# Kernel optimization log

Hardware: AMD Instinct MI355X
Metric: run time of the kernel (lower is better)

Reference implementation:

```python
import jax, jax.numpy as jnp
import numpy as np

GRID_SIZE = 5
SPLINE_ORDER = 3
GRID_RANGE = (-1.0, 1.0)
KERNEL = 3
N_CONVS = 8


def make_grid():
    # Matches KANLinear: arange(-K, G+K+1) * h + grid_range[0]
    h = (GRID_RANGE[1] - GRID_RANGE[0]) / GRID_SIZE
    return jnp.arange(-SPLINE_ORDER, GRID_SIZE + SPLINE_ORDER + 1, dtype=jnp.float32) * h + GRID_RANGE[0]


def b_splines(x, grid):
    # x: (..., kk) -> bases: (..., kk, grid_size + spline_order)
    x = x[..., None]
    bases = ((x >= grid[:-1]) & (x < grid[1:])).astype(x.dtype)
    for p in range(1, SPLINE_ORDER + 1):
        left = (x - grid[: -(p + 1)]) / (grid[p:-1] - grid[: -(p + 1)])
        right = (grid[p + 1:] - x) / (grid[p + 1:] - grid[1:-p])
        bases = left * bases[..., :-1] + right * bases[..., 1:]
    return bases


def setup_inputs() -> dict:
    key = jax.random.key(0)
    k1, k2, k3, k4 = jax.random.split(key, 4)
    B, C, H, W = 16, 32, 64, 64
    kk = KERNEL * KERNEL
    S = GRID_SIZE + SPLINE_ORDER  # number of spline coefficients per input
    x = jax.random.normal(k1, (B, C, H, W), jnp.float32)
    base_w = jax.random.normal(k2, (N_CONVS, kk), jnp.float32) * (1.0 / np.sqrt(kk))
    spline_w = jax.random.normal(k3, (N_CONVS, kk, S), jnp.float32) * 0.1
    spline_scaler = jax.random.normal(k4, (N_CONVS, kk), jnp.float32) * (1.0 / np.sqrt(kk))
    return {"x": x, "base_w": base_w, "spline_w": spline_w, "spline_scaler": spline_scaler}


def reference(x, base_w, spline_w, spline_scaler):
    B, C, H, W = x.shape
    kk = KERNEL * KERNEL
    Ho, Wo = H - KERNEL + 1, W - KERNEL + 1  # stride 1, no pad, no dilation
    # im2col: (B, C*kk, Ho, Wo), feature dim ordered (C, kh, kw) like torch Unfold
    patches = jax.lax.conv_general_dilated_patches(x, (KERNEL, KERNEL), (1, 1), "VALID")
    patches = patches.reshape(B, C, kk, Ho * Wo).transpose(0, 1, 3, 2)  # (B,C,L,kk)
    grid = make_grid()
    basis = b_splines(patches, grid)  # (B,C,L,kk,S)
    scaled_w = spline_w * spline_scaler[..., None]  # (n_convs, kk, S)
    base_out = jnp.einsum("bclk,nk->bcnl", jax.nn.silu(patches), base_w)
    spline_out = jnp.einsum("bclks,nks->bcnl", basis, scaled_w)
    # output channel layout: channel*n_convs + kern
    out = (base_out + spline_out).reshape(B, C * N_CONVS, Ho, Wo)
    return out
```

## Files before the change

kernel.cpp:

```cpp
#include <hip/hip_runtime.h>


typedef __attribute__((ext_vector_type(8))) short bf16x8;
typedef __attribute__((ext_vector_type(4))) float f32x4;

constexpr int Hh = 64, Ww = 64;
constexpr int Ho = 62, Wo = 62;
constexpr int L  = Ho * Wo;
constexpr int NC = 8;
constexpr int RPB = 12;
constexpr int SR  = RPB + 2;
constexpr int NSTRIP = 6;
constexpr int NPX = SR * Ww;
constexpr int LDS_PX = NPX + 4;
constexpr int ZQ = LDS_PX * 2;

__global__ __launch_bounds__(64)
void fold_weights(const float* __restrict__ bw, const float* __restrict__ sw,
                  const float* __restrict__ scl, ushort* __restrict__ wf)
{
    const int l = threadIdx.x;
    const int conv = l & 15;
    const int g = l >> 4;
    for (int c = 0; c < 5; c++) {
        const int tap = 2 * c + (g >> 1);
        for (int j = 0; j < 8; j++) {
            const int slot = (g & 1) * 8 + j;
            float v = 0.0f;
            if (conv < 8 && tap < 9) {
                const int m = conv * 9 + tap;
                if (slot == 0)      v = bw[m];
                else if (slot <= 8) v = sw[m * 8 + (slot - 1)] * scl[m];
            }
            wf[(c * 64 + l) * 8 + j] = (ushort)((__float_as_uint(v) + 0x8000u) >> 16);
        }
    }
}

__device__ __forceinline__ uint pk(float lo, float hi) {
    return ((__float_as_uint(lo) + 0x8000u) >> 16) |
           ((__float_as_uint(hi) + 0x8000u) & 0xffff0000u);
}

__global__ __launch_bounds__(256, 4)
void kan_conv_kernel(const float* __restrict__ x,
                     const ushort* __restrict__ wf,
                     float* __restrict__ out)
{
    __shared__ uint4 pix[LDS_PX * 2 + 2];

    const int strip = blockIdx.x % NSTRIP;
    const int bc    = blockIdx.x / NSTRIP;
    const int s0    = strip * RPB;

    if (threadIdx.x < 2) pix[ZQ + threadIdx.x] = make_uint4(0, 0, 0, 0);

    const int stage_rows = (s0 + SR <= Hh) ? SR : (Hh - s0);
    const int npx = stage_rows * Ww;
    const float* xp = x + (size_t)bc * (Hh * Ww) + (size_t)s0 * Ww;

    for (int p = threadIdx.x; p < npx; p += 256) {
        const float v  = xp[p];
        const float sv = v / (1.0f + __expf(-v));

        const float u  = (v + 2.2f) * 2.5f;
        const float fj = floorf(u);
        const float t  = u - fj;
        const int   j  = (int)fj - 3;
        const float om = 1.0f - t;
        const float t2 = t * t;
        const float w3 = t * t2 * (1.0f / 6.0f);
        const float w0 = om * om * om * (1.0f / 6.0f);
        const float w1 = fmaf(t2, fmaf(t, 0.5f, -1.0f), 2.0f / 3.0f);
        const float w2 = 1.0f - w0 - w1 - w3;

        float b[8];
#pragma unroll
        for (int s = 0; s < 8; s++) {
            float r = 0.0f;
            r = (j == s    ) ? w0 : r;
            r = (j == s - 1) ? w1 : r;
            r = (j == s - 2) ? w2 : r;
            r = (j == s - 3) ? w3 : r;
            b[s] = r;
        }

        const int sw_ = (p >> 2) & 1;
        pix[p * 2 + sw_]       = make_uint4(pk(sv, b[0]), pk(b[1], b[2]),
                                            pk(b[3], b[4]), pk(b[5], b[6]));
        pix[p * 2 + (1 - sw_)] = make_uint4(pk(b[7], 0.0f), 0u, 0u, 0u);
    }
    __syncthreads();

    const int wv = threadIdx.x >> 6;
    const int l  = threadIdx.x & 63;
    const int g  = l >> 4;
    const int m  = l & 15;
    const int h  = g & 1;
    const int c0 = wv * 16;

    bf16x8 wa[5];
    const uint4* wfv = (const uint4*)wf;
#pragma unroll
    for (int c = 0; c < 5; c++) {
        uint4 q = wfv[c * 64 + l];
        wa[c] = *(const bf16x8*)&q;
    }

    int dtap[5];
#pragma unroll
    for (int c = 0; c < 5; c++) {
        int tap = 2 * c + (g >> 1);
        if (tap > 8) tap = 8;
        dtap[c] = (tap / 3) * Ww + (tap % 3);
    }

    const int nrt  = (s0 + RPB <= Ho) ? RPB : (Ho - s0);
    const int pcol = c0 + m;
    const char* pixb = (const char*)pix;

    for (int rl = 0; rl < nrt; rl++) {
        const int ptile = rl * Ww + pcol;
        f32x4 acc = {0.0f, 0.0f, 0.0f, 0.0f};
#pragma unroll
        for (int c = 0; c < 5; c++) {
            const int p = ptile + dtap[c];
            int addr = (p << 5) + ((((p >> 2) & 1) ^ h) << 4);
            if (c == 4 && g >= 2) addr = ZQ * 16;
            const bf16x8 bfrag = *(const bf16x8*)(pixb + addr);
            acc = __builtin_amdgcn_mfma_f32_16x16x32_bf16(wa[c], bfrag, acc, 0, 0, 0);
        }

        if (g < 2 && pcol < Wo) {
            float* op = out + ((size_t)bc * NC + g * 4) * L
                            + (size_t)(s0 + rl) * Wo + pcol;
            op[0 * L] = acc.x;
            op[1 * L] = acc.y;
            op[2 * L] = acc.z;
            op[3 * L] = acc.w;
        }
    }
}

extern "C" void kernel_launch(void* const* d_in, const int* in_sizes, int n_in,
                              void* d_out, int out_size, void* d_ws, size_t ws_size,
                              hipStream_t stream) {
    const float* x   = (const float*)d_in[0];
    const float* bw  = (const float*)d_in[1];
    const float* sw  = (const float*)d_in[2];
    const float* scl = (const float*)d_in[3];
    ushort* wf = (ushort*)d_ws;
    float* out = (float*)d_out;

    fold_weights<<<1, 64, 0, stream>>>(bw, sw, scl, wf);

    const int planes = in_sizes[0] / (Hh * Ww);
    dim3 grid(planes * NSTRIP);
    kan_conv_kernel<<<grid, 256, 0, stream>>>(x, wf, out);
}
```

Baseline: 104.9 us.

## Compute two output rows per MFMA tile using the unused half of the M dimension

```diff
diff --git a/kernel.cpp b/kernel.cpp
--- a/kernel.cpp
+++ b/kernel.cpp
@@ -13,24 +13,26 @@
 constexpr int NSTRIP = 6;
 constexpr int NPX = SR * Ww;
 constexpr int LDS_PX = NPX + 4;
-constexpr int ZQ = LDS_PX * 2;
 
 __global__ __launch_bounds__(64)
 void fold_weights(const float* __restrict__ bw, const float* __restrict__ sw,
                   const float* __restrict__ scl, ushort* __restrict__ wf)
 {
     const int l = threadIdx.x;
-    const int conv = l & 15;
+    const int m = l & 15;
     const int g = l >> 4;
-    for (int c = 0; c < 5; c++) {
+    const int conv = m & 7;
+    for (int c = 0; c < 6; c++) {
         const int tap = 2 * c + (g >> 1);
+        const int kh  = tap / 3, kw = tap % 3;
+        const int kh2 = (m < 8) ? kh : kh - 1;
         for (int j = 0; j < 8; j++) {
             const int slot = (g & 1) * 8 + j;
             float v = 0.0f;
-            if (conv < 8 && tap < 9) {
-                const int m = conv * 9 + tap;
-                if (slot == 0)      v = bw[m];
-                else if (slot <= 8) v = sw[m * 8 + (slot - 1)] * scl[m];
+            if (kh2 >= 0 && kh2 <= 2) {
+                const int idx = conv * 9 + kh2 * 3 + kw;
+                if (slot == 0)      v = bw[idx];
+                else if (slot <= 8) v = sw[idx * 8 + (slot - 1)] * scl[idx];
             }
             wf[(c * 64 + l) * 8 + j] = (ushort)((__float_as_uint(v) + 0x8000u) >> 16);
         }
@@ -47,13 +49,11 @@
                      const ushort* __restrict__ wf,
                      float* __restrict__ out)
 {
-    __shared__ uint4 pix[LDS_PX * 2 + 2];
+    __shared__ uint4 pix[LDS_PX * 2];
 
     const int strip = blockIdx.x % NSTRIP;
     const int bc    = blockIdx.x / NSTRIP;
     const int s0    = strip * RPB;
-
-    if (threadIdx.x < 2) pix[ZQ + threadIdx.x] = make_uint4(0, 0, 0, 0);
 
     const int stage_rows = (s0 + SR <= Hh) ? SR : (Hh - s0);
     const int npx = stage_rows * Ww;
@@ -97,43 +97,42 @@
     const int g  = l >> 4;
     const int m  = l & 15;
     const int h  = g & 1;
-    const int c0 = wv * 16;
+    const int pcol = wv * 16 + m;
 
-    bf16x8 wa[5];
+    bf16x8 wa[6];
     const uint4* wfv = (const uint4*)wf;
 #pragma unroll
-    for (int c = 0; c < 5; c++) {
+    for (int c = 0; c < 6; c++) {
         uint4 q = wfv[c * 64 + l];
         wa[c] = *(const bf16x8*)&q;
     }
 
-    int dtap[5];
+    int dtap[6];
 #pragma unroll
-    for (int c = 0; c < 5; c++) {
-        int tap = 2 * c + (g >> 1);
-        if (tap > 8) tap = 8;
+    for (int c = 0; c < 6; c++) {
+        const int tap = 2 * c + (g >> 1);
         dtap[c] = (tap / 3) * Ww + (tap % 3);
     }
 
-    const int nrt  = (s0 + RPB <= Ho) ? RPB : (Ho - s0);
-    const int pcol = c0 + m;
+    const int nrt = (s0 + RPB <= Ho) ? RPB : (Ho - s0);
     const char* pixb = (const char*)pix;
+    const int rowoff = g >> 1;
+    const int cbase  = (g & 1) * 4;
 
-    for (int rl = 0; rl < nrt; rl++) {
+    for (int rl = 0; rl < nrt; rl += 2) {
         const int ptile = rl * Ww + pcol;
         f32x4 acc = {0.0f, 0.0f, 0.0f, 0.0f};
 #pragma unroll
-        for (int c = 0; c < 5; c++) {
+        for (int c = 0; c < 6; c++) {
             const int p = ptile + dtap[c];
-            int addr = (p << 5) + ((((p >> 2) & 1) ^ h) << 4);
-            if (c == 4 && g >= 2) addr = ZQ * 16;
+            const int addr = (p << 5) + ((((p >> 2) & 1) ^ h) << 4);
             const bf16x8 bfrag = *(const bf16x8*)(pixb + addr);
             acc = __builtin_amdgcn_mfma_f32_16x16x32_bf16(wa[c], bfrag, acc, 0, 0, 0);
         }
 
-        if (g < 2 && pcol < Wo) {
-            float* op = out + ((size_t)bc * NC + g * 4) * L
-                            + (size_t)(s0 + rl) * Wo + pcol;
+        if (pcol < Wo) {
+            float* op = out + ((size_t)bc * NC + cbase) * L
+                            + (size_t)(s0 + rl + rowoff) * Wo + pcol;
             op[0 * L] = acc.x;
             op[1 * L] = acc.y;
             op[2 * L] = acc.z;
```

New measurement: 101.3 us. 3.5% less time.
